# Kernel tuning notes

Measured on AMD Instinct MI355X. Metric: run time of the kernel, lower is better.

The kernel has to match this reference:

```python
import jax, jax.numpy as jnp
import numpy as np

D_MODEL, N_HEADS = 1024, 16
HEAD_DIM = D_MODEL // N_HEADS  # 64
BS, Q_LEN, SEQ_LEN = 4, 1024, 1024


def setup_inputs() -> dict:
    key = jax.random.key(0)
    kq, kk, kv, kp, km = jax.random.split(key, 5)
    q = jax.random.normal(kq, (BS, N_HEADS, Q_LEN, HEAD_DIM), dtype=jnp.float32)
    k = jax.random.normal(kk, (BS, N_HEADS, HEAD_DIM, SEQ_LEN), dtype=jnp.float32)
    v = jax.random.normal(kv, (BS, N_HEADS, SEQ_LEN, HEAD_DIM), dtype=jnp.float32)
    prev = jax.random.normal(kp, (BS, N_HEADS, Q_LEN, SEQ_LEN), dtype=jnp.float32)
    attn_weighted_mask = jax.random.uniform(km, (1, N_HEADS, Q_LEN, SEQ_LEN), dtype=jnp.float32)
    scale = jnp.asarray(HEAD_DIM ** (-0.5), dtype=jnp.float32)  # nn.Parameter scalar
    return {"q": q, "k": k, "v": v, "prev": prev,
            "attn_weighted_mask": attn_weighted_mask, "scale": scale}


def reference(q, k, v, prev, attn_weighted_mask, scale):
    # scores = (q @ k) * scale + prev       [bs, h, q_len, seq_len]
    attn_scores = jnp.einsum('bhqd,bhds->bhqs', q, k) * scale + prev
    # softmax over keys; attn_dropout p=0.0 -> identity
    attn_weights = jax.nn.softmax(attn_scores, axis=-1)
    # post-softmax elementwise weighted mask
    attn_weights = attn_weights * attn_weighted_mask
    # output = attn_weights @ v             [bs, h, q_len, d_v]
    output = jnp.einsum('bhqs,bhsd->bhqd', attn_weights, v)
    # res_attention=True -> also return weights and pre-softmax scores
    return output, attn_weights, attn_scores
```

## Files before the change

kernel.cpp:

```cpp
#include <hip/hip_runtime.h>


#define QL 1024
#define SL 1024
#define HD 64

typedef __attribute__((ext_vector_type(8))) short bf16x8;
typedef __attribute__((ext_vector_type(4))) short bf16x4;
typedef __attribute__((ext_vector_type(4))) float f32x4;

__device__ __forceinline__ short f2bf(float f) {
    union { float f; unsigned u; } v; v.f = f;
    unsigned r = v.u + 0x7FFFu + ((v.u >> 16) & 1u);
    return (short)(r >> 16);
}

__global__ __launch_bounds__(256) void _prepack_kv(
    const float* __restrict__ k, const float* __restrict__ v,
    short* __restrict__ ws)
{
    __shared__ short tile[64][72];
    const int t = threadIdx.x;
    int b = blockIdx.x;
    const float* src; short* dst; int ld_src, ld_dst;
    if (b < 1024) {
        const int bh = b >> 4, st = b & 15;
        src = k + (size_t)bh * 65536 + st * 64;               ld_src = 1024;
        dst = ws + (size_t)bh * 65536 + (size_t)st * 4096;    ld_dst = 64;
    } else {
        b -= 1024;
        const int bh = b >> 4, st = b & 15;
        src = v + (size_t)bh * 65536 + (size_t)st * 4096;     ld_src = 64;
        dst = ws + 4194304 + (size_t)bh * 65536 + st * 64;    ld_dst = 1024;
    }
    {
        const int r = t >> 2, c0 = (t & 3) * 16;
#pragma unroll
        for (int i = 0; i < 4; ++i) {
            float4 f = *(const float4*)&src[(size_t)r * ld_src + c0 + 4 * i];
            bf16x4 s4 = { f2bf(f.x), f2bf(f.y), f2bf(f.z), f2bf(f.w) };
            *(bf16x4*)&tile[r][c0 + 4 * i] = s4;
        }
    }
    __syncthreads();
    {
        const int r = t >> 2, c0 = (t & 3) * 16;
        bf16x8 o0, o1;
#pragma unroll
        for (int j = 0; j < 8; ++j) o0[j] = tile[c0 + j][r];
#pragma unroll
        for (int j = 0; j < 8; ++j) o1[j] = tile[c0 + 8 + j][r];
        *(bf16x8*)&dst[(size_t)r * ld_dst + c0]     = o0;
        *(bf16x8*)&dst[(size_t)r * ld_dst + c0 + 8] = o1;
    }
}

__global__ __launch_bounds__(256, 4) void _attn_main(
    const float* __restrict__ q, const float* __restrict__ prev,
    const float* __restrict__ mask, const float* __restrict__ scale_p,
    const short* __restrict__ Kt, const short* __restrict__ Vt,
    float* __restrict__ out)
{
    __shared__ short wbuf[16384];
    __shared__ float red[64];

    const int tid  = threadIdx.x;
    const int w    = tid >> 6;
    const int lane = tid & 63;
    const int quad = lane >> 4;
    const int lp   = lane & 15;

    const int blk = (blockIdx.x & 7) * 512 + (blockIdx.x >> 3);
    const int bh  = blk >> 6;
    const int qt  = blk & 63;
    const int h   = bh & 15;
    const int q0  = qt * 16;

    const float scale = scale_p[0];

    const float* Qb = q    + (size_t)bh * QL * HD + (size_t)q0 * HD;
    const float* Pb = prev + (size_t)bh * QL * SL + (size_t)q0 * SL;
    const float* Mb = mask + (size_t)h  * QL * SL + (size_t)q0 * SL;
    const short* Kb = Kt + (size_t)bh * (SL * HD);
    const short* Vb = Vt + (size_t)bh * (SL * HD);

    float* Ob   = out            + (size_t)bh * QL * HD + (size_t)q0 * HD;
    float* Wout = out + 4194304  + (size_t)bh * QL * SL + (size_t)q0 * SL;
    float* Sout = out + 71303168 + (size_t)bh * QL * SL + (size_t)q0 * SL;

    bf16x8 aq[2];
#pragma unroll
    for (int ks = 0; ks < 2; ++ks) {
        const float* qp = Qb + (size_t)lp * HD + ks * 32 + quad * 8;
        float4 a = *(const float4*)qp;
        float4 b = *(const float4*)(qp + 4);
        aq[ks][0] = f2bf(a.x * scale); aq[ks][1] = f2bf(a.y * scale);
        aq[ks][2] = f2bf(a.z * scale); aq[ks][3] = f2bf(a.w * scale);
        aq[ks][4] = f2bf(b.x * scale); aq[ks][5] = f2bf(b.y * scale);
        aq[ks][6] = f2bf(b.z * scale); aq[ks][7] = f2bf(b.w * scale);
    }

    const int s0 = 256 * w;
    f32x4 acc[16];
#pragma unroll
    for (int t = 0; t < 16; ++t) acc[t] = (f32x4){0.f, 0.f, 0.f, 0.f};
#pragma unroll
    for (int ks = 0; ks < 2; ++ks) {
#pragma unroll
        for (int t = 0; t < 16; ++t) {
            bf16x8 bk = *(const bf16x8*)&Kb[(size_t)(s0 + 16 * t + lp) * HD
                                            + ks * 32 + quad * 8];
            acc[t] = __builtin_amdgcn_mfma_f32_16x16x32_bf16(aq[ks], bk, acc[t], 0, 0, 0);
        }
    }

    float lsum[4] = {0.f, 0.f, 0.f, 0.f};
#pragma unroll
    for (int t = 0; t < 16; ++t) {
#pragma unroll
        for (int r = 0; r < 4; ++r) {
            const int row = quad * 4 + r;
            const int col = s0 + 16 * t + lp;
            float sv = acc[t][r] + Pb[(size_t)row * SL + col];
            Sout[(size_t)row * SL + col] = sv;
            float e = __expf(sv);
            acc[t][r] = e;
            lsum[r] += e;
        }
    }
#pragma unroll
    for (int r = 0; r < 4; ++r) {
        float s = lsum[r];
        s += __shfl_xor(s, 1);  s += __shfl_xor(s, 2);
        s += __shfl_xor(s, 4);  s += __shfl_xor(s, 8);
        lsum[r] = s;
    }
    if (lp == 0) {
#pragma unroll
        for (int r = 0; r < 4; ++r) red[w * 16 + quad * 4 + r] = lsum[r];
    }
    __syncthreads();
    float rinv[4];
#pragma unroll
    for (int r = 0; r < 4; ++r) {
        float s = red[0 * 16 + quad * 4 + r] + red[1 * 16 + quad * 4 + r]
                + red[2 * 16 + quad * 4 + r] + red[3 * 16 + quad * 4 + r];
        rinv[r] = 1.0f / s;
    }

#pragma unroll
    for (int t = 0; t < 16; ++t) {
#pragma unroll
        for (int r = 0; r < 4; ++r) {
            const int row = quad * 4 + r;
            const int col = s0 + 16 * t + lp;
            float wv = acc[t][r] * rinv[r] * Mb[(size_t)row * SL + col];
            Wout[(size_t)row * SL + col] = wv;
            wbuf[(((col >> 3) * 16) + row) * 8 + (lp & 7)] = f2bf(wv);
        }
    }
    __syncthreads();

    f32x4 oacc = {0.f, 0.f, 0.f, 0.f};
#pragma unroll 4
    for (int ks = 0; ks < 32; ++ks) {
        bf16x8 aw = *(const bf16x8*)&wbuf[((ks * 4 + quad) * 16 + lp) * 8];
        bf16x8 bv = *(const bf16x8*)&Vb[(size_t)(16 * w + lp) * SL
                                        + ks * 32 + quad * 8];
        oacc = __builtin_amdgcn_mfma_f32_16x16x32_bf16(aw, bv, oacc, 0, 0, 0);
    }
#pragma unroll
    for (int r = 0; r < 4; ++r)
        Ob[(size_t)(quad * 4 + r) * HD + 16 * w + lp] = oacc[r];
}

__global__ __launch_bounds__(256) void _attn_fallback(
    const float* __restrict__ q, const float* __restrict__ k,
    const float* __restrict__ v, const float* __restrict__ prev,
    const float* __restrict__ mask, const float* __restrict__ scale_p,
    float* __restrict__ out)
{
    const int WSTR = SL + 8;
    __shared__ short wbuf[16 * (SL + 8)];
    __shared__ float red[4 * 16];

    const int tid  = threadIdx.x;
    const int w    = tid >> 6;
    const int lane = tid & 63;
    const int quad = lane >> 4;
    const int lp   = lane & 15;

    const int blk = blockIdx.x;
    const int bh  = blk >> 6;
    const int qt  = blk & 63;
    const int h   = bh & 15;
    const int q0  = qt * 16;

    const float scale = scale_p[0];

    const float* Qb = q    + (size_t)bh * QL * HD + (size_t)q0 * HD;
    const float* Kb = k    + (size_t)bh * HD * SL;
    const float* Vb = v    + (size_t)bh * SL * HD;
    const float* Pb = prev + (size_t)bh * QL * SL + (size_t)q0 * SL;
    const float* Mb = mask + (size_t)h  * QL * SL + (size_t)q0 * SL;

    float* Ob   = out            + (size_t)bh * QL * HD + (size_t)q0 * HD;
    float* Wout = out + 4194304  + (size_t)bh * QL * SL + (size_t)q0 * SL;
    float* Sout = out + 71303168 + (size_t)bh * QL * SL + (size_t)q0 * SL;

    bf16x8 aq[2];
#pragma unroll
    for (int ks = 0; ks < 2; ++ks) {
        const float* qp = Qb + (size_t)lp * HD + ks * 32 + quad * 8;
#pragma unroll
        for (int j = 0; j < 8; ++j) aq[ks][j] = f2bf(qp[j] * scale);
    }

    const int s0 = 256 * w;
    f32x4 acc[16];
#pragma unroll
    for (int t = 0; t < 16; ++t) {
#pragma unroll
        for (int r = 0; r < 4; ++r)
            acc[t][r] = Pb[(size_t)(quad * 4 + r) * SL + s0 + 16 * t + lp];
    }
#pragma unroll
    for (int ks = 0; ks < 2; ++ks) {
#pragma unroll
        for (int t = 0; t < 16; ++t) {
            bf16x8 bk;
            const float* kp = Kb + (size_t)(ks * 32 + quad * 8) * SL + s0 + 16 * t + lp;
#pragma unroll
            for (int j = 0; j < 8; ++j) bk[j] = f2bf(kp[(size_t)j * SL]);
            acc[t] = __builtin_amdgcn_mfma_f32_16x16x32_bf16(aq[ks], bk, acc[t], 0, 0, 0);
        }
    }

    float lsum[4] = {0.f, 0.f, 0.f, 0.f};
#pragma unroll
    for (int t = 0; t < 16; ++t) {
#pragma unroll
        for (int r = 0; r < 4; ++r) {
            float sv = acc[t][r];
            Sout[(size_t)(quad * 4 + r) * SL + s0 + 16 * t + lp] = sv;
            float e = __expf(sv);
            acc[t][r] = e;
            lsum[r] += e;
        }
    }
#pragma unroll
    for (int r = 0; r < 4; ++r) {
        float s = lsum[r];
        s += __shfl_xor(s, 1);  s += __shfl_xor(s, 2);
        s += __shfl_xor(s, 4);  s += __shfl_xor(s, 8);
        lsum[r] = s;
    }
    if (lp == 0) {
#pragma unroll
        for (int r = 0; r < 4; ++r) red[w * 16 + quad * 4 + r] = lsum[r];
    }
    __syncthreads();
    float rinv[4];
#pragma unroll
    for (int r = 0; r < 4; ++r) {
        float s = red[0 * 16 + quad * 4 + r] + red[1 * 16 + quad * 4 + r]
                + red[2 * 16 + quad * 4 + r] + red[3 * 16 + quad * 4 + r];
        rinv[r] = 1.0f / s;
    }

#pragma unroll
    for (int t = 0; t < 16; ++t) {
#pragma unroll
        for (int r = 0; r < 4; ++r) {
            int row = quad * 4 + r;
            int col = s0 + 16 * t + lp;
            float wv = acc[t][r] * rinv[r] * Mb[(size_t)row * SL + col];
            Wout[(size_t)row * SL + col] = wv;
            wbuf[row * WSTR + col] = f2bf(wv);
        }
    }
    __syncthreads();

    f32x4 oacc = {0.f, 0.f, 0.f, 0.f};
#pragma unroll 4
    for (int ks = 0; ks < 32; ++ks) {
        bf16x8 aw = *(const bf16x8*)&wbuf[lp * WSTR + ks * 32 + quad * 8];
        bf16x8 bv;
        const float* vp = Vb + (size_t)(ks * 32 + quad * 8) * HD + 16 * w + lp;
#pragma unroll
        for (int j = 0; j < 8; ++j) bv[j] = f2bf(vp[(size_t)j * HD]);
        oacc = __builtin_amdgcn_mfma_f32_16x16x32_bf16(aw, bv, oacc, 0, 0, 0);
    }
#pragma unroll
    for (int r = 0; r < 4; ++r)
        Ob[(size_t)(quad * 4 + r) * HD + 16 * w + lp] = oacc[r];
}

extern "C" void kernel_launch(void* const* d_in, const int* in_sizes, int n_in,
                              void* d_out, int out_size, void* d_ws, size_t ws_size,
                              hipStream_t stream) {
    const float* q     = (const float*)d_in[0];
    const float* k     = (const float*)d_in[1];
    const float* v     = (const float*)d_in[2];
    const float* prev  = (const float*)d_in[3];
    const float* mask  = (const float*)d_in[4];
    const float* scale = (const float*)d_in[5];
    float* out = (float*)d_out;

    if (d_ws != nullptr && ws_size >= (size_t)16 * 1024 * 1024) {
        short* ws = (short*)d_ws;
        _prepack_kv<<<dim3(2048), dim3(256), 0, stream>>>(k, v, ws);
        _attn_main<<<dim3(4096), dim3(256), 0, stream>>>(
            q, prev, mask, scale, ws, ws + 4194304, out);
    } else {
        _attn_fallback<<<dim3(4096), dim3(256), 0, stream>>>(
            q, k, v, prev, mask, scale, out);
    }
}
```

Before: 941.3 us.

## Double threads per block, split key columns and PV reduction across 8 waves

Raises the attention block from 4 to 8 waves. Each wave now handles 128 key columns instead of 256, and the softmax row-sum reduction is widened to 8 partials. The PV product is split into two halves over the key dimension, combined through a shared-memory buffer. The prev tile is also loaded straight into the MFMA accumulators before the QK product, so the bias load is issued early and the separate add goes away. This halves per-thread register pressure and raises the number of loads in flight. The cost is an extra barrier and extra shared memory for the partial output sums.

```diff
diff --git a/kernel.cpp b/kernel.cpp
--- a/kernel.cpp
+++ b/kernel.cpp
@@ -55,14 +55,15 @@
     }
 }
 
-__global__ __launch_bounds__(256, 4) void _attn_main(
+__global__ __launch_bounds__(512, 8) void _attn_main(
     const float* __restrict__ q, const float* __restrict__ prev,
     const float* __restrict__ mask, const float* __restrict__ scale_p,
     const short* __restrict__ Kt, const short* __restrict__ Vt,
     float* __restrict__ out)
 {
     __shared__ short wbuf[16384];
-    __shared__ float red[64];
+    __shared__ float red[128];
+    __shared__ float obuf[1024];
 
     const int tid  = threadIdx.x;
     const int w    = tid >> 6;
@@ -87,6 +88,16 @@
     float* Ob   = out            + (size_t)bh * QL * HD + (size_t)q0 * HD;
     float* Wout = out + 4194304  + (size_t)bh * QL * SL + (size_t)q0 * SL;
     float* Sout = out + 71303168 + (size_t)bh * QL * SL + (size_t)q0 * SL;
+
+    const int s0 = 128 * w;
+
+    f32x4 acc[8];
+#pragma unroll
+    for (int t = 0; t < 8; ++t) {
+#pragma unroll
+        for (int r = 0; r < 4; ++r)
+            acc[t][r] = Pb[(size_t)(quad * 4 + r) * SL + s0 + 16 * t + lp];
+    }
 
     bf16x8 aq[2];
 #pragma unroll
@@ -100,14 +111,10 @@
         aq[ks][6] = f2bf(b.z * scale); aq[ks][7] = f2bf(b.w * scale);
     }
 
-    const int s0 = 256 * w;
-    f32x4 acc[16];
-#pragma unroll
-    for (int t = 0; t < 16; ++t) acc[t] = (f32x4){0.f, 0.f, 0.f, 0.f};
 #pragma unroll
     for (int ks = 0; ks < 2; ++ks) {
 #pragma unroll
-        for (int t = 0; t < 16; ++t) {
+        for (int t = 0; t < 8; ++t) {
             bf16x8 bk = *(const bf16x8*)&Kb[(size_t)(s0 + 16 * t + lp) * HD
                                             + ks * 32 + quad * 8];
             acc[t] = __builtin_amdgcn_mfma_f32_16x16x32_bf16(aq[ks], bk, acc[t], 0, 0, 0);
@@ -116,12 +123,12 @@
 
     float lsum[4] = {0.f, 0.f, 0.f, 0.f};
 #pragma unroll
-    for (int t = 0; t < 16; ++t) {
+    for (int t = 0; t < 8; ++t) {
 #pragma unroll
         for (int r = 0; r < 4; ++r) {
             const int row = quad * 4 + r;
             const int col = s0 + 16 * t + lp;
-            float sv = acc[t][r] + Pb[(size_t)row * SL + col];
+            float sv = acc[t][r];
             Sout[(size_t)row * SL + col] = sv;
             float e = __expf(sv);
             acc[t][r] = e;
@@ -143,13 +150,14 @@
     float rinv[4];
 #pragma unroll
     for (int r = 0; r < 4; ++r) {
-        float s = red[0 * 16 + quad * 4 + r] + red[1 * 16 + quad * 4 + r]
-                + red[2 * 16 + quad * 4 + r] + red[3 * 16 + quad * 4 + r];
+        float s = 0.f;
+#pragma unroll
+        for (int u = 0; u < 8; ++u) s += red[u * 16 + quad * 4 + r];
         rinv[r] = 1.0f / s;
     }
 
 #pragma unroll
-    for (int t = 0; t < 16; ++t) {
+    for (int t = 0; t < 8; ++t) {
 #pragma unroll
         for (int r = 0; r < 4; ++r) {
             const int row = quad * 4 + r;
@@ -161,17 +169,29 @@
     }
     __syncthreads();
 
+    const int dgrp = w & 3;
+    const int kh   = w >> 2;
     f32x4 oacc = {0.f, 0.f, 0.f, 0.f};
-#pragma unroll 4
-    for (int ks = 0; ks < 32; ++ks) {
+#pragma unroll 8
+    for (int kk = 0; kk < 16; ++kk) {
+        const int ks = kh * 16 + kk;
         bf16x8 aw = *(const bf16x8*)&wbuf[((ks * 4 + quad) * 16 + lp) * 8];
-        bf16x8 bv = *(const bf16x8*)&Vb[(size_t)(16 * w + lp) * SL
+        bf16x8 bv = *(const bf16x8*)&Vb[(size_t)(16 * dgrp + lp) * SL
                                         + ks * 32 + quad * 8];
         oacc = __builtin_amdgcn_mfma_f32_16x16x32_bf16(aw, bv, oacc, 0, 0, 0);
     }
-#pragma unroll
-    for (int r = 0; r < 4; ++r)
-        Ob[(size_t)(quad * 4 + r) * HD + 16 * w + lp] = oacc[r];
+    if (kh == 1) {
+#pragma unroll
+        for (int r = 0; r < 4; ++r)
+            obuf[(quad * 4 + r) * 64 + 16 * dgrp + lp] = oacc[r];
+    }
+    __syncthreads();
+    if (kh == 0) {
+#pragma unroll
+        for (int r = 0; r < 4; ++r)
+            Ob[(size_t)(quad * 4 + r) * HD + 16 * dgrp + lp]
+                = oacc[r] + obuf[(quad * 4 + r) * 64 + 16 * dgrp + lp];
+    }
 }
 
 __global__ __launch_bounds__(256) void _attn_fallback(
@@ -310,7 +330,7 @@
     if (d_ws != nullptr && ws_size >= (size_t)16 * 1024 * 1024) {
         short* ws = (short*)d_ws;
         _prepack_kv<<<dim3(2048), dim3(256), 0, stream>>>(k, v, ws);
-        _attn_main<<<dim3(4096), dim3(256), 0, stream>>>(
+        _attn_main<<<dim3(4096), dim3(512), 0, stream>>>(
             q, prev, mask, scale, ws, ws + 4194304, out);
     } else {
         _attn_fallback<<<dim3(4096), dim3(256), 0, stream>>>(
```

Result: slower. 983.6 us (+4.5%).
